# Optimization experiments

Hardware: AMD Instinct MI355X
Metric: run time of the kernel (lower is better)

The kernel has to match this reference:

```python
import jax, jax.numpy as jnp
import numpy as np

D_MODEL = 256
N_HEADS = 8
D_HEAD = D_MODEL // N_HEADS
B = 65536
LN_EPS = 1e-5


def setup_inputs() -> dict:
    key = jax.random.key(0)
    ks = jax.random.split(key, 6)
    s = 1.0 / np.sqrt(D_MODEL)
    x = jax.random.normal(ks[0], (B, D_MODEL), dtype=jnp.float32)
    Wq = jax.random.normal(ks[1], (D_MODEL, D_MODEL), dtype=jnp.float32) * s
    Wk = jax.random.normal(ks[2], (D_MODEL, D_MODEL), dtype=jnp.float32) * s
    Wv = jax.random.normal(ks[3], (D_MODEL, D_MODEL), dtype=jnp.float32) * s
    Wout = jax.random.normal(ks[4], (D_MODEL, D_MODEL), dtype=jnp.float32) * s
    b_out = jnp.zeros((D_MODEL,), dtype=jnp.float32)
    # L initialized to identity per head (matches nn.init.eye_) plus tiny noise
    L = jnp.broadcast_to(jnp.eye(D_HEAD, dtype=jnp.float32), (N_HEADS, D_HEAD, D_HEAD)) \
        + 0.01 * jax.random.normal(ks[5], (N_HEADS, D_HEAD, D_HEAD), dtype=jnp.float32)
    gamma = jnp.ones((D_MODEL,), dtype=jnp.float32)
    beta = jnp.zeros((D_MODEL,), dtype=jnp.float32)
    return {"x": x, "Wq": Wq, "Wk": Wk, "Wv": Wv, "Wout": Wout,
            "b_out": b_out, "L": L, "gamma": gamma, "beta": beta}


def reference(x, Wq, Wk, Wv, Wout, b_out, L, gamma, beta):
    b = x.shape[0]
    # projections; view as [B, H, d_head]
    Q = (x @ Wq).reshape(b, N_HEADS, D_HEAD)
    K = (x @ Wk).reshape(b, N_HEADS, D_HEAD)
    V = (x @ Wv).reshape(b, N_HEADS, D_HEAD)
    # pairwise head differences: [B, Hq, Hk, d_head]
    diff = Q[:, :, None, :] - K[:, None, :, :]
    # per-key-head learned metric transform: L indexed by key head
    diff_t = jnp.einsum('bqkd,kdf->bqkf', diff, L)
    sq_dist = jnp.sum(diff_t * diff_t, axis=-1)            # [B, Hq, Hk]
    attn = jax.nn.softmax(-sq_dist / jnp.sqrt(jnp.float32(D_HEAD)), axis=2)
    out = jnp.einsum('bqk,bkd->bqd', attn, V).reshape(b, D_MODEL)
    out = out @ Wout + b_out
    h = out + x
    # LayerNorm over last dim
    mu = jnp.mean(h, axis=-1, keepdims=True)
    var = jnp.mean((h - mu) ** 2, axis=-1, keepdims=True)
    return (h - mu) * jax.lax.rsqrt(var + LN_EPS) * gamma + beta
```

## Files before the change

### kernel.cpp

```cpp
#include <hip/hip_runtime.h>


typedef __bf16 bf16x8 __attribute__((ext_vector_type(8)));
typedef float  f32x4  __attribute__((ext_vector_type(4)));
typedef int    i32x4  __attribute__((ext_vector_type(4)));
typedef int    i32x2  __attribute__((ext_vector_type(2)));
typedef unsigned short u16;

__device__ __forceinline__ float bf2f(u16 u){
  unsigned int x = ((unsigned int)u) << 16;
  return __builtin_bit_cast(float, x);
}
__device__ __forceinline__ u16 f2bf(float f){
  unsigned int u = __builtin_bit_cast(unsigned int, f);
  u += 0x7FFFu + ((u >> 16) & 1u);
  return (u16)(u >> 16);
}
__device__ __forceinline__ unsigned int pk2(float lo, float hi){
  return ((unsigned int)f2bf(hi) << 16) | (unsigned int)f2bf(lo);
}
__device__ __forceinline__ bf16x8 ldfrag_lds(const u16* p){
  return __builtin_bit_cast(bf16x8, *(const i32x4*)p);
}
__device__ __forceinline__ bf16x8 ldfrag_g(const u16* p){
  return __builtin_bit_cast(bf16x8, *(const i32x4*)p);
}

#define LROW 264

__device__ __forceinline__ int kts_off(int k, int r, int fb){
  return (k*2048 + r*64 + fb*2) ^ ((r & 7) << 4);
}

__global__ __launch_bounds__(256) void geo_prep(
    const float* __restrict__ Wq, const float* __restrict__ Wk,
    const float* __restrict__ Wv, const float* __restrict__ Wout,
    const float* __restrict__ L, u16* __restrict__ ws)
{
  const int b = blockIdx.x, t = threadIdx.x;
  if (b < 64){
    const int m = b >> 4;
    const float* src = (m == 0) ? Wq : (m == 1) ? Wk : (m == 2) ? Wv : Wout;
    u16* dstbase = (m < 3) ? (ws + m*65536) : (ws + 196608);
    const int tile = b & 15;
    const int tr = tile >> 2, tc = tile & 3;
    __shared__ float tlf[64][68];
    {
      const int row = t >> 2, cs = (t & 3)*16;
      #pragma unroll
      for (int j = 0; j < 4; ++j){
        f32x4 v = *(const f32x4*)(src + (size_t)(tr*64 + row)*256 + tc*64 + cs + j*4);
        #pragma unroll
        for (int p = 0; p < 4; ++p) tlf[row][cs + j*4 + p] = v[p];
      }
    }
    __syncthreads();
    {
      const int n = t >> 2, cs = (t & 3)*16;
      float us[16];
      if (m == 1){
        const int hh = n >> 5, f = n & 31;
        const int kg = tc*2 + hh;
        #pragma unroll
        for (int j = 0; j < 16; ++j) us[j] = 0.f;
        #pragma unroll 4
        for (int d = 0; d < 32; ++d){
          const float lv = L[kg*1024 + d*32 + f];
          #pragma unroll
          for (int j = 0; j < 16; ++j)
            us[j] = fmaf(tlf[cs + j][hh*32 + d], lv, us[j]);
        }
      } else {
        #pragma unroll
        for (int j = 0; j < 16; ++j) us[j] = tlf[cs + j][n];
      }
      #pragma unroll
      for (int h = 0; h < 2; ++h){
        i32x4 o;
        #pragma unroll
        for (int p = 0; p < 4; ++p)
          o[p] = (int)pk2(us[h*8 + 2*p], us[h*8 + 2*p + 1]);
        *(i32x4*)(dstbase + (size_t)(tc*64 + n)*256 + tr*64 + cs + h*8) = o;
      }
    }
  } else {
    u16* Lt = ws + 262144;
    const int k = t >> 5, f = t & 31;
    for (int d = 0; d < 32; ++d)
      Lt[k*1024 + f*32 + d] = f2bf(L[k*1024 + d*32 + f]);
  }
}

__global__ __launch_bounds__(512, 6) void geo_fused(
    const float* __restrict__ x,     const u16* __restrict__ WqkvT,
    const u16* __restrict__ WoutT,   const u16* __restrict__ Lt,
    const float* __restrict__ b_out, const float* __restrict__ gamma,
    const float* __restrict__ beta,  float* __restrict__ out)
{
  __shared__ __align__(16) char pool[50688];
  u16*  xsU  = (u16*)(pool);
  char* ktsB = pool;
  u16*  hsU  = (u16*)(pool);
  u16*  QsU  = (u16*)(pool + 16896);
  u16*  aoU  = (u16*)(pool + 16896);
  u16*  VsU  = (u16*)(pool + 33792);

  const int t    = threadIdx.x;
  const int lane = t & 63;
  const int w    = t >> 6;
  const int l15  = lane & 15;
  const int quad = lane >> 4;
  const long rowbase = (long)blockIdx.x * 32;

  {
    const int r  = t >> 4;
    const int c0 = (t & 15) * 16;
    const float* src = x + (rowbase + r)*256 + c0;
    unsigned int wds[8];
    #pragma unroll
    for (int j = 0; j < 4; ++j){
      f32x4 v = *(const f32x4*)(src + j*4);
      wds[j*2    ] = pk2(v[0], v[1]);
      wds[j*2 + 1] = pk2(v[2], v[3]);
    }
    #pragma unroll
    for (int h = 0; h < 2; ++h){
      i32x4 o;
      #pragma unroll
      for (int p = 0; p < 4; ++p) o[p] = (int)wds[h*4 + p];
      *(i32x4*)&xsU[r*LROW + c0 + h*8] = o;
    }
  }
  __syncthreads();

  #pragma unroll
  for (int si = 0; si < 2; ++si){
    const int s = si << 1;
    const u16* Bbase = WqkvT + (size_t)(s*256 + w*32)*256;
    u16* dst = si ? VsU : QsU;
    f32x4 acc[2][2];
    #pragma unroll
    for (int mt = 0; mt < 2; ++mt)
      #pragma unroll
      for (int nt = 0; nt < 2; ++nt) acc[mt][nt] = f32x4{0.f,0.f,0.f,0.f};
    #pragma unroll
    for (int kk = 0; kk < 8; ++kk){
      const int c0 = kk*32 + quad*8;
      bf16x8 a[2], bb[2];
      #pragma unroll
      for (int mt = 0; mt < 2; ++mt) a[mt] = ldfrag_lds(&xsU[(mt*16 + l15)*LROW + c0]);
      #pragma unroll
      for (int nt = 0; nt < 2; ++nt) bb[nt] = ldfrag_g(Bbase + (size_t)(nt*16 + l15)*256 + c0);
      #pragma unroll
      for (int mt = 0; mt < 2; ++mt)
        #pragma unroll
        for (int nt = 0; nt < 2; ++nt)
          acc[mt][nt] = __builtin_amdgcn_mfma_f32_16x16x32_bf16(a[mt], bb[nt], acc[mt][nt], 0, 0, 0);
    }
    #pragma unroll
    for (int mt = 0; mt < 2; ++mt)
      #pragma unroll
      for (int nt = 0; nt < 2; ++nt){
        const int col = w*32 + nt*16 + l15;
        #pragma unroll
        for (int reg = 0; reg < 4; ++reg)
          dst[(mt*16 + quad*4 + reg)*LROW + col] = f2bf(acc[mt][nt][reg]);
      }
  }

  f32x4 kacc[2][2];
  {
    #pragma unroll
    for (int mt = 0; mt < 2; ++mt)
      #pragma unroll
      for (int nt = 0; nt < 2; ++nt) kacc[mt][nt] = f32x4{0.f,0.f,0.f,0.f};
    const u16* Abase = WqkvT + (size_t)(256 + w*32)*256;
    #pragma unroll
    for (int kk = 0; kk < 8; ++kk){
      const int c0 = kk*32 + quad*8;
      bf16x8 aW[2], bX[2];
      #pragma unroll
      for (int mt = 0; mt < 2; ++mt) aW[mt] = ldfrag_g(Abase + (size_t)(mt*16 + l15)*256 + c0);
      #pragma unroll
      for (int nt = 0; nt < 2; ++nt) bX[nt] = ldfrag_lds(&xsU[(nt*16 + l15)*LROW + c0]);
      #pragma unroll
      for (int mt = 0; mt < 2; ++mt)
        #pragma unroll
        for (int nt = 0; nt < 2; ++nt)
          kacc[mt][nt] = __builtin_amdgcn_mfma_f32_16x16x32_bf16(aW[mt], bX[nt], kacc[mt][nt], 0, 0, 0);
    }
  }
  __syncthreads();

  {
    #pragma unroll
    for (int mt = 0; mt < 2; ++mt)
      #pragma unroll
      for (int nt = 0; nt < 2; ++nt){
        const int r = nt*16 + l15;
        i32x2 o;
        o[0] = (int)pk2(kacc[mt][nt][0], kacc[mt][nt][1]);
        o[1] = (int)pk2(kacc[mt][nt][2], kacc[mt][nt][3]);
        *(i32x2*)(ktsB + kts_off(w, r, mt*16 + quad*4)) = o;
      }
  }
  __syncthreads();

  float lg[2][8];
  {
    bf16x8 bQ[2];
    #pragma unroll
    for (int nt = 0; nt < 2; ++nt)
      bQ[nt] = ldfrag_lds(&QsU[(nt*16 + l15)*LROW + w*32 + quad*8]);
    #pragma unroll
    for (int k = 0; k < 8; ++k){
      bf16x8 aL[2];
      #pragma unroll
      for (int mt = 0; mt < 2; ++mt)
        aL[mt] = ldfrag_g(Lt + k*1024 + (mt*16 + l15)*32 + quad*8);
      f32x4 acc[2][2];
      #pragma unroll
      for (int mt = 0; mt < 2; ++mt)
        #pragma unroll
        for (int nt = 0; nt < 2; ++nt)
          acc[mt][nt] = __builtin_amdgcn_mfma_f32_16x16x32_bf16(aL[mt], bQ[nt],
                          f32x4{0.f,0.f,0.f,0.f}, 0, 0, 0);
      #pragma unroll
      for (int nt = 0; nt < 2; ++nt){
        const int r = nt*16 + l15;
        float s = 0.f;
        #pragma unroll
        for (int mt = 0; mt < 2; ++mt){
          i32x2 kt2 = *(const i32x2*)(ktsB + kts_off(k, r, mt*16 + quad*4));
          unsigned int u0 = (unsigned int)kt2[0], u1 = (unsigned int)kt2[1];
          float kv0 = __builtin_bit_cast(float, u0 << 16);
          float kv1 = __builtin_bit_cast(float, u0 & 0xFFFF0000u);
          float kv2 = __builtin_bit_cast(float, u1 << 16);
          float kv3 = __builtin_bit_cast(float, u1 & 0xFFFF0000u);
          float d0 = acc[mt][nt][0] - kv0, d1 = acc[mt][nt][1] - kv1;
          float d2 = acc[mt][nt][2] - kv2, d3 = acc[mt][nt][3] - kv3;
          s = fmaf(d0, d0, s); s = fmaf(d1, d1, s);
          s = fmaf(d2, d2, s); s = fmaf(d3, d3, s);
        }
        s += __shfl_xor(s, 16);
        s += __shfl_xor(s, 32);
        lg[nt][k] = s * -0.17677669529663687f;
      }
    }
  }
  __syncthreads();

  {
    #pragma unroll
    for (int nt = 0; nt < 2; ++nt){
      const int r = nt*16 + l15;
      float mx = lg[nt][0];
      #pragma unroll
      for (int k = 1; k < 8; ++k) mx = fmaxf(mx, lg[nt][k]);
      float e[8], sum = 0.f;
      #pragma unroll
      for (int k = 0; k < 8; ++k){ e[k] = __expf(lg[nt][k] - mx); sum += e[k]; }
      const float inv = 1.0f / sum;
      float o[8] = {0.f,0.f,0.f,0.f,0.f,0.f,0.f,0.f};
      #pragma unroll
      for (int k = 0; k < 8; ++k){
        i32x4 v = *(const i32x4*)&VsU[r*LROW + k*32 + quad*8];
        const float a = e[k] * inv;
        #pragma unroll
        for (int p = 0; p < 4; ++p){
          unsigned int u = (unsigned int)v[p];
          o[2*p    ] = fmaf(a, __builtin_bit_cast(float, u << 16),         o[2*p    ]);
          o[2*p + 1] = fmaf(a, __builtin_bit_cast(float, u & 0xFFFF0000u), o[2*p + 1]);
        }
      }
      i32x4 pkv;
      #pragma unroll
      for (int p = 0; p < 4; ++p) pkv[p] = (int)pk2(o[2*p], o[2*p + 1]);
      *(i32x4*)&aoU[r*LROW + w*32 + quad*8] = pkv;
    }
  }
  __syncthreads();

  {
    f32x4 acc[2][2];
    #pragma unroll
    for (int mt = 0; mt < 2; ++mt)
      #pragma unroll
      for (int nt = 0; nt < 2; ++nt) acc[mt][nt] = f32x4{0.f,0.f,0.f,0.f};
    #pragma unroll
    for (int kk = 0; kk < 8; ++kk){
      const int c0 = kk*32 + quad*8;
      bf16x8 a[2], bb[2];
      #pragma unroll
      for (int mt = 0; mt < 2; ++mt) a[mt] = ldfrag_lds(&aoU[(mt*16 + l15)*LROW + c0]);
      #pragma unroll
      for (int nt = 0; nt < 2; ++nt)
        bb[nt] = ldfrag_g(WoutT + (size_t)(w*32 + nt*16 + l15)*256 + c0);
      #pragma unroll
      for (int mt = 0; mt < 2; ++mt)
        #pragma unroll
        for (int nt = 0; nt < 2; ++nt)
          acc[mt][nt] = __builtin_amdgcn_mfma_f32_16x16x32_bf16(a[mt], bb[nt], acc[mt][nt], 0, 0, 0);
    }
    #pragma unroll
    for (int nt = 0; nt < 2; ++nt){
      const int col = w*32 + nt*16 + l15;
      const float bo = b_out[col];
      #pragma unroll
      for (int mt = 0; mt < 2; ++mt)
        #pragma unroll
        for (int reg = 0; reg < 4; ++reg)
          hsU[(mt*16 + quad*4 + reg)*LROW + col] = f2bf(acc[mt][nt][reg] + bo);
    }
  }
  __syncthreads();

  {
    #pragma unroll
    for (int rr = 0; rr < 4; ++rr){
      const int r = w*4 + rr;
      const int c = lane*4;
      i32x2 h2 = *(const i32x2*)&hsU[r*LROW + c];
      f32x4 xv = *(const f32x4*)(x + (rowbase + r)*256 + c);
      unsigned int u0 = (unsigned int)h2[0], u1 = (unsigned int)h2[1];
      f32x4 hv;
      hv[0] = __builtin_bit_cast(float, u0 << 16)         + xv[0];
      hv[1] = __builtin_bit_cast(float, u0 & 0xFFFF0000u) + xv[1];
      hv[2] = __builtin_bit_cast(float, u1 << 16)         + xv[2];
      hv[3] = __builtin_bit_cast(float, u1 & 0xFFFF0000u) + xv[3];
      float s  = hv[0] + hv[1] + hv[2] + hv[3];
      float s2 = hv[0]*hv[0] + hv[1]*hv[1] + hv[2]*hv[2] + hv[3]*hv[3];
      #pragma unroll
      for (int off = 1; off < 64; off <<= 1){
        s  += __shfl_xor(s,  off);
        s2 += __shfl_xor(s2, off);
      }
      const float mu  = s  * (1.0f/256.0f);
      const float var = s2 * (1.0f/256.0f) - mu*mu;
      const float rs  = rsqrtf(var + 1e-5f);
      f32x4 gv = *(const f32x4*)(gamma + c);
      f32x4 bv = *(const f32x4*)(beta  + c);
      f32x4 y;
      y[0] = (hv[0] - mu)*rs*gv[0] + bv[0];
      y[1] = (hv[1] - mu)*rs*gv[1] + bv[1];
      y[2] = (hv[2] - mu)*rs*gv[2] + bv[2];
      y[3] = (hv[3] - mu)*rs*gv[3] + bv[3];
      *(f32x4*)(out + (rowbase + r)*256 + c) = y;
    }
  }
}

extern "C" void kernel_launch(void* const* d_in, const int* in_sizes, int n_in,
                              void* d_out, int out_size, void* d_ws, size_t ws_size,
                              hipStream_t stream)
{
  const float* x     = (const float*)d_in[0];
  const float* Wq    = (const float*)d_in[1];
  const float* Wk    = (const float*)d_in[2];
  const float* Wv    = (const float*)d_in[3];
  const float* Wout  = (const float*)d_in[4];
  const float* b_out = (const float*)d_in[5];
  const float* L     = (const float*)d_in[6];
  const float* gamma = (const float*)d_in[7];
  const float* beta  = (const float*)d_in[8];
  u16* ws = (u16*)d_ws;

  geo_prep<<<65, 256, 0, stream>>>(Wq, Wk, Wv, Wout, L, ws);
  geo_fused<<<2048, 512, 0, stream>>>(x, ws, ws + 196608, ws + 262144,
                                      b_out, gamma, beta, (float*)d_out);
}
```

Before: 261.9 us.

## Transpose MFMA operands for packed LDS stores, drop a barrier, widen LayerNorm

The Q/V and output projections now put the weights in the A operand and the activations in the B operand, so each lane holds consecutive columns of one row. Results can then be written to LDS as packed 8-byte bf16 stores instead of scalar 2-byte stores, and the output bias is loaded once as vectors up front. The barrier between the logits stage and the softmax stage is removed. LayerNorm now has each lane handle 16 elements of a row, so one wave covers four rows at once with a 4-step shuffle reduction instead of 6 steps per row. Removing the barrier risks a race, because the softmax output buffer aliases the Q buffer.

Result: slower. 284.5 us (+8.6%).

```diff
diff --git a/kernel.cpp b/kernel.cpp
--- a/kernel.cpp
+++ b/kernel.cpp
@@ -7,10 +7,6 @@
 typedef int    i32x2  __attribute__((ext_vector_type(2)));
 typedef unsigned short u16;
 
-__device__ __forceinline__ float bf2f(u16 u){
-  unsigned int x = ((unsigned int)u) << 16;
-  return __builtin_bit_cast(float, x);
-}
 __device__ __forceinline__ u16 f2bf(float f){
   unsigned int u = __builtin_bit_cast(unsigned int, f);
   u += 0x7FFFu + ((u >> 16) & 1u);
@@ -112,6 +108,9 @@
   const int quad = lane >> 4;
   const long rowbase = (long)blockIdx.x * 32;
 
+  const f32x4 bo0 = *(const f32x4*)(b_out + w*32 + quad*4);
+  const f32x4 bo1 = *(const f32x4*)(b_out + w*32 + 16 + quad*4);
+
   {
     const int r  = t >> 4;
     const int c0 = (t & 15) * 16;
@@ -136,7 +135,7 @@
   #pragma unroll
   for (int si = 0; si < 2; ++si){
     const int s = si << 1;
-    const u16* Bbase = WqkvT + (size_t)(s*256 + w*32)*256;
+    const u16* Abase = WqkvT + (size_t)(s*256 + w*32)*256;
     u16* dst = si ? VsU : QsU;
     f32x4 acc[2][2];
     #pragma unroll
@@ -146,25 +145,26 @@
     #pragma unroll
     for (int kk = 0; kk < 8; ++kk){
       const int c0 = kk*32 + quad*8;
-      bf16x8 a[2], bb[2];
-      #pragma unroll
-      for (int mt = 0; mt < 2; ++mt) a[mt] = ldfrag_lds(&xsU[(mt*16 + l15)*LROW + c0]);
-      #pragma unroll
-      for (int nt = 0; nt < 2; ++nt) bb[nt] = ldfrag_g(Bbase + (size_t)(nt*16 + l15)*256 + c0);
+      bf16x8 aW[2], bX[2];
+      #pragma unroll
+      for (int mt = 0; mt < 2; ++mt) aW[mt] = ldfrag_g(Abase + (size_t)(mt*16 + l15)*256 + c0);
+      #pragma unroll
+      for (int nt = 0; nt < 2; ++nt) bX[nt] = ldfrag_lds(&xsU[(nt*16 + l15)*LROW + c0]);
       #pragma unroll
       for (int mt = 0; mt < 2; ++mt)
         #pragma unroll
         for (int nt = 0; nt < 2; ++nt)
-          acc[mt][nt] = __builtin_amdgcn_mfma_f32_16x16x32_bf16(a[mt], bb[nt], acc[mt][nt], 0, 0, 0);
+          acc[mt][nt] = __builtin_amdgcn_mfma_f32_16x16x32_bf16(aW[mt], bX[nt], acc[mt][nt], 0, 0, 0);
     }
     #pragma unroll
     for (int mt = 0; mt < 2; ++mt)
       #pragma unroll
       for (int nt = 0; nt < 2; ++nt){
-        const int col = w*32 + nt*16 + l15;
-        #pragma unroll
-        for (int reg = 0; reg < 4; ++reg)
-          dst[(mt*16 + quad*4 + reg)*LROW + col] = f2bf(acc[mt][nt][reg]);
+        const int r = nt*16 + l15;
+        i32x2 o;
+        o[0] = (int)pk2(acc[mt][nt][0], acc[mt][nt][1]);
+        o[1] = (int)pk2(acc[mt][nt][2], acc[mt][nt][3]);
+        *(i32x2*)&dst[r*LROW + w*32 + mt*16 + quad*4] = o;
       }
   }
 
@@ -248,7 +248,6 @@
       }
     }
   }
-  __syncthreads();
 
   {
     #pragma unroll
@@ -290,62 +289,75 @@
     #pragma unroll
     for (int kk = 0; kk < 8; ++kk){
       const int c0 = kk*32 + quad*8;
-      bf16x8 a[2], bb[2];
-      #pragma unroll
-      for (int mt = 0; mt < 2; ++mt) a[mt] = ldfrag_lds(&aoU[(mt*16 + l15)*LROW + c0]);
-      #pragma unroll
-      for (int nt = 0; nt < 2; ++nt)
-        bb[nt] = ldfrag_g(WoutT + (size_t)(w*32 + nt*16 + l15)*256 + c0);
+      bf16x8 aW[2], bA[2];
+      #pragma unroll
+      for (int mt = 0; mt < 2; ++mt)
+        aW[mt] = ldfrag_g(WoutT + (size_t)(w*32 + mt*16 + l15)*256 + c0);
+      #pragma unroll
+      for (int nt = 0; nt < 2; ++nt) bA[nt] = ldfrag_lds(&aoU[(nt*16 + l15)*LROW + c0]);
       #pragma unroll
       for (int mt = 0; mt < 2; ++mt)
         #pragma unroll
         for (int nt = 0; nt < 2; ++nt)
-          acc[mt][nt] = __builtin_amdgcn_mfma_f32_16x16x32_bf16(a[mt], bb[nt], acc[mt][nt], 0, 0, 0);
+          acc[mt][nt] = __builtin_amdgcn_mfma_f32_16x16x32_bf16(aW[mt], bA[nt], acc[mt][nt], 0, 0, 0);
     }
     #pragma unroll
     for (int nt = 0; nt < 2; ++nt){
-      const int col = w*32 + nt*16 + l15;
-      const float bo = b_out[col];
-      #pragma unroll
-      for (int mt = 0; mt < 2; ++mt)
-        #pragma unroll
-        for (int reg = 0; reg < 4; ++reg)
-          hsU[(mt*16 + quad*4 + reg)*LROW + col] = f2bf(acc[mt][nt][reg] + bo);
-    }
-  }
-  __syncthreads();
-
-  {
-    #pragma unroll
-    for (int rr = 0; rr < 4; ++rr){
-      const int r = w*4 + rr;
-      const int c = lane*4;
-      i32x2 h2 = *(const i32x2*)&hsU[r*LROW + c];
-      f32x4 xv = *(const f32x4*)(x + (rowbase + r)*256 + c);
-      unsigned int u0 = (unsigned int)h2[0], u1 = (unsigned int)h2[1];
-      f32x4 hv;
-      hv[0] = __builtin_bit_cast(float, u0 << 16)         + xv[0];
-      hv[1] = __builtin_bit_cast(float, u0 & 0xFFFF0000u) + xv[1];
-      hv[2] = __builtin_bit_cast(float, u1 << 16)         + xv[2];
-      hv[3] = __builtin_bit_cast(float, u1 & 0xFFFF0000u) + xv[3];
-      float s  = hv[0] + hv[1] + hv[2] + hv[3];
-      float s2 = hv[0]*hv[0] + hv[1]*hv[1] + hv[2]*hv[2] + hv[3]*hv[3];
-      #pragma unroll
-      for (int off = 1; off < 64; off <<= 1){
-        s  += __shfl_xor(s,  off);
-        s2 += __shfl_xor(s2, off);
-      }
-      const float mu  = s  * (1.0f/256.0f);
-      const float var = s2 * (1.0f/256.0f) - mu*mu;
-      const float rs  = rsqrtf(var + 1e-5f);
-      f32x4 gv = *(const f32x4*)(gamma + c);
-      f32x4 bv = *(const f32x4*)(beta  + c);
+      const int r = nt*16 + l15;
+      {
+        i32x2 o;
+        o[0] = (int)pk2(acc[0][nt][0] + bo0[0], acc[0][nt][1] + bo0[1]);
+        o[1] = (int)pk2(acc[0][nt][2] + bo0[2], acc[0][nt][3] + bo0[3]);
+        *(i32x2*)&hsU[r*LROW + w*32 + quad*4] = o;
+      }
+      {
+        i32x2 o;
+        o[0] = (int)pk2(acc[1][nt][0] + bo1[0], acc[1][nt][1] + bo1[1]);
+        o[1] = (int)pk2(acc[1][nt][2] + bo1[2], acc[1][nt][3] + bo1[3]);
+        *(i32x2*)&hsU[r*LROW + w*32 + 16 + quad*4] = o;
+      }
+    }
+  }
+  __syncthreads();
+
+  {
+    const int r  = w*4 + quad;
+    const int c0 = l15*16;
+    i32x4 h0 = *(const i32x4*)&hsU[r*LROW + c0];
+    i32x4 h1 = *(const i32x4*)&hsU[r*LROW + c0 + 8];
+    const float* xr = x + (rowbase + r)*256 + c0;
+    float hv[16];
+    #pragma unroll
+    for (int p = 0; p < 4; ++p){
+      f32x4 xv = *(const f32x4*)(xr + p*4);
+      unsigned int ua = (unsigned int)((p < 2) ? h0[p*2]     : h1[(p-2)*2]);
+      unsigned int ub = (unsigned int)((p < 2) ? h0[p*2 + 1] : h1[(p-2)*2 + 1]);
+      hv[p*4 + 0] = __builtin_bit_cast(float, ua << 16)          + xv[0];
+      hv[p*4 + 1] = __builtin_bit_cast(float, ua & 0xFFFF0000u)  + xv[1];
+      hv[p*4 + 2] = __builtin_bit_cast(float, ub << 16)          + xv[2];
+      hv[p*4 + 3] = __builtin_bit_cast(float, ub & 0xFFFF0000u)  + xv[3];
+    }
+    float s = 0.f, s2 = 0.f;
+    #pragma unroll
+    for (int i = 0; i < 16; ++i){ s += hv[i]; s2 = fmaf(hv[i], hv[i], s2); }
+    #pragma unroll
+    for (int off = 1; off < 16; off <<= 1){
+      s  += __shfl_xor(s,  off);
+      s2 += __shfl_xor(s2, off);
+    }
+    const float mu  = s  * (1.0f/256.0f);
+    const float var = s2 * (1.0f/256.0f) - mu*mu;
+    const float rs  = rsqrtf(var + 1e-5f);
+    float* orow = out + (rowbase + r)*256 + c0;
+    #pragma unroll
+    for (int p = 0; p < 4; ++p){
+      f32x4 gv = *(const f32x4*)(gamma + c0 + p*4);
+      f32x4 bv = *(const f32x4*)(beta  + c0 + p*4);
       f32x4 y;
-      y[0] = (hv[0] - mu)*rs*gv[0] + bv[0];
-      y[1] = (hv[1] - mu)*rs*gv[1] + bv[1];
-      y[2] = (hv[2] - mu)*rs*gv[2] + bv[2];
-      y[3] = (hv[3] - mu)*rs*gv[3] + bv[3];
-      *(f32x4*)(out + (rowbase + r)*256 + c) = y;
+      #pragma unroll
+      for (int q = 0; q < 4; ++q)
+        y[q] = (hv[p*4 + q] - mu)*rs*gv[q] + bv[q];
+      *(f32x4*)(orow + p*4) = y;
     }
   }
 }
```
